# Kernel optimization log

Hardware: AMD Instinct MI355X
Metric: run time of the kernel (lower is better)

Reference implementation:

```python
import jax, jax.numpy as jnp
import numpy as np

NUM_CLASSES = 5
FEATURES = 256      # self.features_num
DIRECTIONS = 10000  # self.directions_num
H = 128
W = 128
LOSS_WEIGHT = 1.0


def setup_inputs() -> dict:
    key = jax.random.key(0)
    k1, k2, k3 = jax.random.split(key, 3)
    feature = jax.random.normal(k1, (1, FEATURES, H, W), dtype=jnp.float32)
    label = jax.random.randint(k2, (1, 1, H, W), 0, NUM_CLASSES, dtype=jnp.int32)
    proj_mat = jax.random.normal(k3, (DIRECTIONS, FEATURES), dtype=jnp.float32)
    # __init__ normalizes each row to unit norm
    proj_mat = proj_mat / jnp.sqrt((proj_mat ** 2).sum(axis=1, keepdims=True))
    return {"feature": feature, "label": label, "proj_mat": proj_mat}


def _class_loss(feat2d, w, proj_mat):
    # feat2d: [F, N] features, w: [N] {0,1} mask for this class, proj_mat: [D, F]
    n = w.sum()
    n_safe = jnp.maximum(n, 1.0)
    # first/second moments over the masked pixels (detached in the original via .cpu().numpy())
    miu = (feat2d @ w) / n_safe                                  # [F]
    m2mat = ((feat2d * w[None, :]) @ feat2d.T) / n_safe          # [F, F]
    cov_eps = jnp.clip(1e-8 * 1000.0 / n_safe, 1e-8, 1e-5)
    cov = m2mat - jnp.outer(miu, miu) + cov_eps * jnp.eye(FEATURES, dtype=feat2d.dtype)
    cov = jax.lax.stop_gradient(cov)  # original computes eig on detached numpy cov
    evals, evecs = jnp.linalg.eigh(cov)  # cov symmetric -> eigh (original: np.linalg.eig + sort)
    order = jnp.argsort(evals)[::-1]
    evals = jnp.maximum(evals[order], 1e-12)
    evecs = evecs[:, order]
    # per-direction variance after projection; rows of proj_mat already unit norm
    pm = proj_mat / jnp.sqrt((proj_mat ** 2).sum(axis=1, keepdims=True))
    std = jnp.sqrt((pm ** 2) @ evals)                            # [D]
    centered = feat2d - jax.lax.stop_gradient(miu)[:, None]      # miu_curr_t is detached
    # feat_vecs = proj_mat @ (evecs.T @ centered) / std  -> [D, N], the big intermediate
    fp = ((pm @ evecs.T) @ centered) / std[:, None]
    # masked moment accumulation (only class pixels contribute)
    m2 = ((fp ** 2) @ w) / n_safe                                # [D]
    m4 = ((fp ** 4) @ w) / n_safe                                # [D]
    loss_m2 = jnp.mean((m2 - 1.0) ** 2)
    loss_kurt = jnp.mean((m4 - 3.0 * m2 ** 2) ** 2)  # Gaussian target: m4 = 3*m2^2
    active = (n > 0).astype(feat2d.dtype)
    return loss_m2, loss_kurt, active


def reference(feature, label, proj_mat):
    feat2d = feature[0].reshape(FEATURES, H * W)    # [F, N]
    lbl = label[0, 0].reshape(H * W)                # [N]
    total = jnp.zeros((), dtype=feature.dtype)
    active_num = jnp.zeros((), dtype=feature.dtype)
    for c in range(1, NUM_CLASSES):  # original skips class 0 (background)
        w = (lbl == c).astype(feature.dtype)
        lm2, lk, a = _class_loss(feat2d, w, proj_mat)
        total = total + a * (lm2 + lk)
        active_num = active_num + a
    return LOSS_WEIGHT * total / jnp.maximum(active_num, 1.0)
```

## Files before the change

kernel.cpp:

```cpp
#include <hip/hip_runtime.h>
#include <cstdint>
#include <cstddef>

#define FEAT 256
#define HWPX 16384
#define NDIR 10000
#define NCLS 4
#define BCAP 4096
#define NSWO 7
#define JTOL 4e-12f
#define NBLK_FP 157
#define NRND (NSWO*63)

static const size_t OFF_FEATT = 0;
static const size_t OFF_IDX   = OFF_FEATT + (size_t)HWPX*FEAT;
static const size_t OFF_CNT   = OFF_IDX + (size_t)NCLS*HWPX;
static const size_t OFF_MIU   = OFF_CNT + 64;
static const size_t OFF_MIUP  = OFF_MIU + (size_t)NCLS*FEAT;
static const size_t OFF_G     = OFF_MIUP + (size_t)32*NCLS*FEAT;
static const size_t OFF_ETS   = OFF_G + (size_t)NCLS*FEAT*FEAT;
static const size_t OFF_EVAL  = OFF_ETS + (size_t)NCLS*FEAT*FEAT;
static const size_t OFF_LPART = OFF_EVAL + (size_t)NCLS*FEAT;
static const size_t OFF_B     = OFF_LPART + (size_t)NCLS*160*2;
static const size_t OFF_XCH   = OFF_B + (size_t)NCLS*FEAT*BCAP;

#define XCH_STRIDE  ((size_t)131072)
#define XCH_PIN_OFF 65536
#define XCH_FLG_OFF (65536 + 1024)

__device__ __forceinline__ float wsum64(float v){
  int x;
  x = __builtin_amdgcn_update_dpp(0, __float_as_int(v), 0x121, 0xF, 0xF, false); v += __int_as_float(x);
  x = __builtin_amdgcn_update_dpp(0, __float_as_int(v), 0x122, 0xF, 0xF, false); v += __int_as_float(x);
  x = __builtin_amdgcn_update_dpp(0, __float_as_int(v), 0x124, 0xF, 0xF, false); v += __int_as_float(x);
  x = __builtin_amdgcn_update_dpp(0, __float_as_int(v), 0x128, 0xF, 0xF, false); v += __int_as_float(x);
  float a = __int_as_float(__builtin_amdgcn_readlane(__float_as_int(v), 0));
  float b = __int_as_float(__builtin_amdgcn_readlane(__float_as_int(v), 16));
  float c = __int_as_float(__builtin_amdgcn_readlane(__float_as_int(v), 32));
  float d = __int_as_float(__builtin_amdgcn_readlane(__float_as_int(v), 48));
  return (a + b) + (c + d);
}

__device__ __forceinline__ void sysst(float* p, float v){
  __hip_atomic_store(p, v, __ATOMIC_RELAXED, __HIP_MEMORY_SCOPE_SYSTEM);
}
__device__ __forceinline__ float sysld(const float* p){
  return __hip_atomic_load(p, __ATOMIC_RELAXED, __HIP_MEMORY_SCOPE_SYSTEM);
}
__device__ __forceinline__ void syssti(int* p, int v){
  __hip_atomic_store(p, v, __ATOMIC_RELAXED, __HIP_MEMORY_SCOPE_SYSTEM);
}
__device__ __forceinline__ int sysldi(const int* p){
  return __hip_atomic_load(p, __ATOMIC_RELAXED, __HIP_MEMORY_SCOPE_SYSTEM);
}
__device__ __forceinline__ void waitflag(int* f, int val){
  while (sysldi(f) < val) __builtin_amdgcn_s_sleep(1);
  asm volatile("" ::: "memory");
}

__global__ __launch_bounds__(256) void k_transpose(const float* __restrict__ feat, float* __restrict__ ws){
  __shared__ float tile[32][33];
  float* featT = ws + OFF_FEATT;
  int j0 = blockIdx.x*32, f0 = blockIdx.y*32;
  int tx = threadIdx.x, ty = threadIdx.y;
  #pragma unroll
  for (int r=0;r<4;r++){
    int f = f0 + ty + r*8;
    tile[ty+r*8][tx] = feat[(size_t)f*HWPX + j0 + tx];
  }
  __syncthreads();
  #pragma unroll
  for (int r=0;r<4;r++){
    int j = j0 + ty + r*8;
    featT[(size_t)j*FEAT + f0 + tx] = tile[tx][ty+r*8];
  }
}

__global__ __launch_bounds__(256) void k_index(const int* __restrict__ lab, float* ws){
  __shared__ int sc[256];
  int* idx = (int*)(ws + OFF_IDX);
  int* cnt = (int*)(ws + OFF_CNT);
  int t = threadIdx.x;
  if (t < 160){
    #pragma unroll
    for (int cc=0; cc<NCLS; cc++){
      int* fb = (int*)(ws + OFF_XCH + (size_t)cc*XCH_STRIDE + XCH_FLG_OFF);
      fb[t] = 0;
    }
  }
  int base = t*64;
  for (int c=1;c<=NCLS;c++){
    __syncthreads();
    int m = 0;
    for (int k=0;k<64;k++) m += (lab[base+k]==c) ? 1 : 0;
    sc[t] = m;
    __syncthreads();
    for (int off=1; off<256; off<<=1){
      int v = (t>=off)? sc[t-off] : 0;
      __syncthreads();
      sc[t] += v;
      __syncthreads();
    }
    int pos = sc[t] - m;
    if (t==255) cnt[c-1] = sc[255];
    int* ic = idx + (size_t)(c-1)*HWPX;
    for (int k=0;k<64;k++){
      if (lab[base+k]==c) ic[pos++] = base+k;
    }
  }
}

__global__ __launch_bounds__(256) void k_miu_part(const int* __restrict__ lab, float* ws){
  const float* featT = ws + OFF_FEATT;
  float* part = ws + OFF_MIUP;
  int f = threadIdx.x;
  int b = blockIdx.x;
  int j0 = b*512;
  float a0=0.f,a1=0.f,a2=0.f,a3=0.f;
  for (int j=j0;j<j0+512;j++){
    float v = featT[(size_t)j*FEAT + f];
    int c = lab[j];
    a0 += (c==1)? v : 0.f;
    a1 += (c==2)? v : 0.f;
    a2 += (c==3)? v : 0.f;
    a3 += (c==4)? v : 0.f;
  }
  float* pb = part + (size_t)b*NCLS*FEAT;
  pb[0*FEAT+f] = a0;
  pb[1*FEAT+f] = a1;
  pb[2*FEAT+f] = a2;
  pb[3*FEAT+f] = a3;
}

__global__ __launch_bounds__(1024) void k_miu_fin(float* ws){
  int t = threadIdx.x;
  int c = t / FEAT;
  const float* part = ws + OFF_MIUP;
  float s = 0.f;
  for (int b=0;b<32;b++) s += part[(size_t)b*NCLS*FEAT + t];
  int n = ((int*)(ws+OFF_CNT))[c];
  float nf = fmaxf((float)n, 1.f);
  ws[OFF_MIU + t] = s / nf;
}

__global__ __launch_bounds__(256) void k_cov(float* ws){
  __shared__ float Xa[32][68];
  __shared__ float Xb[32][68];
  const float* featT = ws + OFF_FEATT;
  int c = blockIdx.y;
  const int* idx = (const int*)(ws + OFF_IDX) + (size_t)c*HWPX;
  int n = ((int*)(ws+OFF_CNT))[c];
  float nf = fmaxf((float)n,1.f);
  const float* miu = ws + OFF_MIU + (size_t)c*FEAT;
  float* G = ws + OFF_G + (size_t)c*FEAT*FEAT;
  int fb = (blockIdx.x & 3)*64, gb = (blockIdx.x >> 2)*64;
  int t = threadIdx.x;
  int ti = t & 15, tj = t >> 4;
  float acc[4][4] = {};
  int jr = t >> 3;
  int s8 = (t & 7) * 8;
  int nch = (n + 31)/32;
  for (int ch=0; ch<nch; ch++){
    int jg = ch*32 + jr;
    __syncthreads();
    if (jg < n){
      int jx = idx[jg];
      const float* row = featT + (size_t)jx*FEAT;
      #pragma unroll
      for (int k=0;k<8;k++){ Xa[jr][s8+k] = row[fb+s8+k]; Xb[jr][s8+k] = row[gb+s8+k]; }
    } else {
      #pragma unroll
      for (int k=0;k<8;k++){ Xa[jr][s8+k] = 0.f; Xb[jr][s8+k] = 0.f; }
    }
    __syncthreads();
    for (int jj=0;jj<32;jj++){
      float4 av = *(const float4*)&Xa[jj][ti*4];
      float4 bv = *(const float4*)&Xb[jj][tj*4];
      float aa[4] = {av.x,av.y,av.z,av.w};
      float bb[4] = {bv.x,bv.y,bv.z,bv.w};
      #pragma unroll
      for (int ii=0; ii<4; ii++)
        #pragma unroll
        for (int j2=0; j2<4; j2++)
          acc[ii][j2] += aa[ii]*bb[j2];
    }
  }
  float eps = fminf(fmaxf(1e-5f/nf, 1e-8f), 1e-5f);
  #pragma unroll
  for (int ii=0; ii<4; ii++){
    #pragma unroll
    for (int j2=0; j2<4; j2++){
      int f = fb + ti*4 + ii, g = gb + tj*4 + j2;
      float v = acc[ii][j2]/nf - miu[f]*miu[g] + ((f==g)? eps : 0.f);
      G[(size_t)g*FEAT + f] = v;
    }
  }
}

__global__ __launch_bounds__(64) void k_jacobi(float* ws){
  int c = blockIdx.y;
  int w = blockIdx.x;
  float* G    = ws + OFF_G + (size_t)c*FEAT*FEAT;
  float* XC   = ws + OFF_XCH + (size_t)c*XCH_STRIDE;
  float* QIN  = XC;
  float* PIN  = XC + XCH_PIN_OFF;
  float* csqg = XC + XCH_PIN_OFF;
  int*   flg  = (int*)(XC + XCH_FLG_OFF);
  int* dP = flg;       int* crP = flg+32;
  int* dQ = flg+64;    int* crQ = flg+96;
  int* bar = flg+128;
  int lane = threadIdx.x;
  int lane4 = lane*4;

#define FORJ8(M) M(0) M(1) M(2) M(3) M(4) M(5) M(6) M(7)

#define DECL(j) float C##j##x, C##j##y, C##j##z, C##j##w;
  FORJ8(DECL)
#undef DECL
  float n0,n1,n2,n3,n4,n5,n6,n7;

  int pg = (w==0)? 63 : w;
  int qg = (w==0)? 0  : 63 - w;

#define LDP(j) { float4 v_ = *(const float4*)&G[(size_t)(pg*4+(j))*FEAT + lane4]; \
                 C##j##x=v_.x; C##j##y=v_.y; C##j##z=v_.z; C##j##w=v_.w; }
  LDP(0) LDP(1) LDP(2) LDP(3)
#undef LDP
#define LDQ(j) { float4 v_ = *(const float4*)&G[(size_t)(qg*4+((j)-4))*FEAT + lane4]; \
                 C##j##x=v_.x; C##j##y=v_.y; C##j##z=v_.z; C##j##w=v_.w; }
  LDQ(4) LDQ(5) LDQ(6) LDQ(7)
#undef LDQ

#define RG(g,ax,ay,az,aw)  ax=C##g##x; ay=C##g##y; az=C##g##z; aw=C##g##w;
#define WRG(g,ax,ay,az,aw) C##g##x=ax; C##g##y=ay; C##g##z=az; C##g##w=aw;
#define NRM(j) n##j = wsum64(C##j##x*C##j##x + C##j##y*C##j##y + C##j##z*C##j##z + C##j##w*C##j##w);

#define ROTG(ga,gb) { \
    float ax,ay,az,aw,bx,by,bz,bw; \
    RG(ga,ax,ay,az,aw) \
    RG(gb,bx,by,bz,bw) \
    float dp = ax*bx + ay*by + az*bz + aw*bw; \
    float d = wsum64(dp); \
    float na = n##ga, nb = n##gb; \
    bool doit = (d*d > na*nb*JTOL); \
    float tau = (nb - na) * 0.5f * __builtin_amdgcn_rcpf(d); \
    float tt = copysignf(__builtin_amdgcn_rcpf(fabsf(tau) + __builtin_amdgcn_sqrtf(1.f + tau*tau)), tau); \
    float cc = __builtin_amdgcn_rsqf(1.f + tt*tt); \
    float sn = tt*cc; \
    cc = doit ? cc : 1.f; \
    sn = doit ? sn : 0.f; \
    float x_; \
    x_ = ax; ax = cc*x_ - sn*bx; bx = sn*x_ + cc*bx; \
    x_ = ay; ay = cc*x_ - sn*by; by = sn*x_ + cc*by; \
    x_ = az; az = cc*x_ - sn*bz; bz = sn*x_ + cc*bz; \
    x_ = aw; aw = cc*x_ - sn*bw; bw = sn*x_ + cc*bw; \
    float cc2 = cc*cc, sn2 = sn*sn, csd = 2.f*cc*sn*d; \
    n##ga = cc2*na - csd + sn2*nb; \
    n##gb = sn2*na + csd + cc2*nb; \
    WRG(ga,ax,ay,az,aw) \
    WRG(gb,bx,by,bz,bw) \
  }

#define STC(d_, j) { float* p_ = (d_) + ((j)&3)*256 + lane4; \
    sysst(p_+0, C##j##x); sysst(p_+1, C##j##y); sysst(p_+2, C##j##z); sysst(p_+3, C##j##w); }
#define LDC(s_, j) { const float* p_ = (s_) + ((j)&3)*256 + lane4; \
    C##j##x=sysld(p_+0); C##j##y=sysld(p_+1); C##j##z=sysld(p_+2); C##j##w=sysld(p_+3); }

  bool hasP = (w>=1 && w<=30);
  float* pubPdst = (w==1)? QIN : PIN + (size_t)(w-1)*2048;
  int*   pubPd   = (w==1)? (dQ+0) : (dP+(w-1));
  int*   pubPcr  = (w==1)? (crQ+0) : (crP+(w-1));

#pragma clang loop unroll(disable)
  for (int R=0; R<NRND; R++){
    NRM(0) NRM(1) NRM(2) NRM(3) NRM(4) NRM(5) NRM(6) NRM(7)
    ROTG(0,4) ROTG(1,5) ROTG(2,6) ROTG(3,7)
    ROTG(0,5) ROTG(1,6) ROTG(2,7) ROTG(3,4)
    ROTG(0,6) ROTG(1,7) ROTG(2,4) ROTG(3,5)
    ROTG(0,7) ROTG(1,4) ROTG(2,5) ROTG(3,6)
    if ((R & 3) == 3){
      ROTG(3,0) ROTG(1,2)  ROTG(7,4) ROTG(5,6)
      ROTG(3,1) ROTG(2,0)  ROTG(7,5) ROTG(6,4)
      ROTG(3,2) ROTG(0,1)  ROTG(7,6) ROTG(4,5)
    }

    int sl = (R+1) & 1;
    if (w >= 1) waitflag(pubPcr, R-1);
    if (w <= 30) waitflag(crQ+(w+1), R-1);
    if (w >= 1){
      float* db = pubPdst + sl*1024;
      STC(db,0) STC(db,1) STC(db,2) STC(db,3)
    }
    if (w <= 30){
      float* db = QIN + (size_t)(w+1)*2048 + sl*1024;
      STC(db,4) STC(db,5) STC(db,6) STC(db,7)
    }
    asm volatile("s_waitcnt vmcnt(0)" ::: "memory");
    if (w >= 1) syssti(pubPd, R+1);
    if (w <= 30) syssti(dQ+(w+1), R+1);
    if (w == 31){
      C0x=C4x; C0y=C4y; C0z=C4z; C0w=C4w;
      C1x=C5x; C1y=C5y; C1z=C5z; C1w=C5w;
      C2x=C6x; C2y=C6y; C2z=C6z; C2w=C6w;
      C3x=C7x; C3y=C7y; C3z=C7z; C3w=C7w;
    }
    if (hasP) waitflag(dP+w, R+1);
    waitflag(dQ+w, R+1);
    if (hasP){
      const float* sb = PIN + (size_t)w*2048 + sl*1024;
      LDC(sb,0) LDC(sb,1) LDC(sb,2) LDC(sb,3)
    }
    {
      const float* sb = QIN + (size_t)w*2048 + sl*1024;
      LDC(sb,4) LDC(sb,5) LDC(sb,6) LDC(sb,7)
    }
    asm volatile("s_waitcnt vmcnt(0)" ::: "memory");
    if (hasP) syssti(crP+w, R+1);
    syssti(crQ+w, R+1);
  }

  NRM(0) NRM(1) NRM(2) NRM(3) NRM(4) NRM(5) NRM(6) NRM(7)
  int pcol = pg*4, qcol = qg*4;
#define WCSP(j) if (lane == (j)) sysst(&csqg[pcol+(j)], n##j);
#define WCSQ(j) if (lane == (j)) sysst(&csqg[qcol+(j)-4], n##j);
  WCSP(0) WCSP(1) WCSP(2) WCSP(3) WCSQ(4) WCSQ(5) WCSQ(6) WCSQ(7)
#undef WCSP
#undef WCSQ
  asm volatile("s_waitcnt vmcnt(0)" ::: "memory");
  if (lane == 0) __hip_atomic_fetch_add(bar, 1, __ATOMIC_RELAXED, __HIP_MEMORY_SCOPE_SYSTEM);
  while (sysldi(bar) < 32) __builtin_amdgcn_s_sleep(1);
  asm volatile("" ::: "memory");
  float q0 = sysld(&csqg[lane4+0]);
  float q1 = sysld(&csqg[lane4+1]);
  float q2 = sysld(&csqg[lane4+2]);
  float q3 = sysld(&csqg[lane4+3]);
  int u0 = lane4, u1 = lane4+1, u2 = lane4+2, u3 = lane4+3;
  float* evals = ws + OFF_EVAL + (size_t)c*FEAT;
  float* Et = ws + OFF_ETS + (size_t)c*FEAT*FEAT;
#define RANKWR(j, X) { \
    float nv = n##j; \
    float cnt = (((q0>nv)||(q0==nv&&u0<(X)))?1.f:0.f) + (((q1>nv)||(q1==nv&&u1<(X)))?1.f:0.f) \
              + (((q2>nv)||(q2==nv&&u2<(X)))?1.f:0.f) + (((q3>nv)||(q3==nv&&u3<(X)))?1.f:0.f); \
    int rk = (int)wsum64(cnt); \
    if (lane == 0) evals[rk] = sqrtf(nv); \
    float iv = 1.f / sqrtf(nv); \
    float4 v_; v_.x=C##j##x*iv; v_.y=C##j##y*iv; v_.z=C##j##z*iv; v_.w=C##j##w*iv; \
    *(float4*)&Et[(size_t)rk*FEAT + lane4] = v_; \
  }
  RANKWR(0, pcol+0) RANKWR(1, pcol+1) RANKWR(2, pcol+2) RANKWR(3, pcol+3)
  RANKWR(4, qcol+0) RANKWR(5, qcol+1) RANKWR(6, qcol+2) RANKWR(7, qcol+3)
#undef RANKWR
#undef ROTG
#undef NRM
#undef RG
#undef WRG
#undef STC
#undef LDC
#undef FORJ8
}

__global__ __launch_bounds__(256) void k_bmat(float* ws){
  __shared__ float Ae[256][68];
  __shared__ float Bc[256][68];
  int c = blockIdx.z;
  int n = ((int*)(ws+OFF_CNT))[c];
  int j0 = blockIdx.x*64;
  if (j0 >= n) return;
  int kb = blockIdx.y*64;
  const float* featT = ws + OFF_FEATT;
  const int* idx = (const int*)(ws + OFF_IDX) + (size_t)c*HWPX;
  const float* miu = ws + OFF_MIU + (size_t)c*FEAT;
  const float* Ets = ws + OFF_ETS + (size_t)c*FEAT*FEAT;
  float* Bg = ws + OFF_B + (size_t)c*FEAT*BCAP;
  int t = threadIdx.x;
  int l4 = t >> 2, sgf = (t & 3)*64;
  {
    const float* Erow = Ets + (size_t)(kb+l4)*FEAT + sgf;
    for (int f=0; f<64; f+=4){
      float4 v = *(const float4*)&Erow[f];
      Ae[sgf+f+0][l4] = v.x; Ae[sgf+f+1][l4] = v.y;
      Ae[sgf+f+2][l4] = v.z; Ae[sgf+f+3][l4] = v.w;
    }
  }
  {
    int jg = j0 + l4;
    if (jg < n){
      const float* Frow = featT + (size_t)idx[jg]*FEAT + sgf;
      const float* mp = miu + sgf;
      for (int f=0; f<64; f+=4){
        float4 v = *(const float4*)&Frow[f];
        Bc[sgf+f+0][l4] = v.x - mp[f+0];
        Bc[sgf+f+1][l4] = v.y - mp[f+1];
        Bc[sgf+f+2][l4] = v.z - mp[f+2];
        Bc[sgf+f+3][l4] = v.w - mp[f+3];
      }
    } else {
      for (int f=0; f<64; f++) Bc[sgf+f][l4] = 0.f;
    }
  }
  __syncthreads();
  int ti = t & 15, tj = t >> 4;
  float acc[4][4] = {};
  for (int f=0; f<FEAT; f+=4){
    #pragma unroll
    for (int ff=0; ff<4; ff++){
      float4 av = *(const float4*)&Ae[f+ff][ti*4];
      float4 bv = *(const float4*)&Bc[f+ff][tj*4];
      float aa[4] = {av.x,av.y,av.z,av.w};
      float bb[4] = {bv.x,bv.y,bv.z,bv.w};
      #pragma unroll
      for (int kk=0;kk<4;kk++)
        #pragma unroll
        for (int jj=0;jj<4;jj++)
          acc[kk][jj] += aa[kk]*bb[jj];
    }
  }
  #pragma unroll
  for (int kk=0; kk<4; kk++){
    float4 o; o.x=acc[kk][0]; o.y=acc[kk][1]; o.z=acc[kk][2]; o.w=acc[kk][3];
    *(float4*)&Bg[(size_t)(kb + ti*4 + kk)*BCAP + j0 + tj*4] = o;
  }
}

__global__ __launch_bounds__(256) void k_fp(const float* __restrict__ pm, float* ws){
  __shared__ float As[256][68];
  __shared__ float Bs[256][68];
  __shared__ float ev[256];
  __shared__ float red[64][17];
  __shared__ float m2s[64];
  __shared__ float m4s[64];
  int c = blockIdx.y;
  int i0 = blockIdx.x*64;
  int n = ((int*)(ws+OFF_CNT))[c];
  float nf = fmaxf((float)n, 1.f);
  const float* evals = ws + OFF_EVAL + (size_t)c*FEAT;
  const float* Bg = ws + OFF_B + (size_t)c*FEAT*BCAP;
  int t = threadIdx.x;
  int l4 = t >> 2;
  {
    int sgf = (t & 3)*64;
    int gi = i0 + l4;
    if (gi < NDIR){
      const float* row = pm + (size_t)gi*FEAT + sgf;
      for (int f=0; f<64; f+=4){
        float4 v = *(const float4*)&row[f];
        As[sgf+f+0][l4] = v.x; As[sgf+f+1][l4] = v.y;
        As[sgf+f+2][l4] = v.z; As[sgf+f+3][l4] = v.w;
      }
    } else {
      for (int f=0; f<64; f++) As[sgf+f][l4] = 0.f;
    }
  }
  if (t < 256) ev[t] = evals[t];
  int ti = t & 15, tj = t >> 4;
  float s2[4] = {0.f,0.f,0.f,0.f};
  float s4[4] = {0.f,0.f,0.f,0.f};
  int nch = (n + 63)/64;
  int sgj = (t & 3)*16;
  for (int ch=0; ch<nch; ch++){
    int j0 = ch*64;
    __syncthreads();
    for (int g=0; g<4; g++){
      int r = l4 + 64*g;
      const float* Brow = Bg + (size_t)r*BCAP + j0 + sgj;
      #pragma unroll
      for (int e=0; e<16; e+=4){
        int j = j0 + sgj + e;
        float4 v;
        if (j + 3 < n) v = *(const float4*)&Brow[e];
        else {
          v.x = (j+0<n)? Brow[e+0] : 0.f;
          v.y = (j+1<n)? Brow[e+1] : 0.f;
          v.z = (j+2<n)? Brow[e+2] : 0.f;
          v.w = (j+3<n)? Brow[e+3] : 0.f;
        }
        *(float4*)&Bs[r][sgj+e] = v;
      }
    }
    __syncthreads();
    float acc[4][4] = {};
    for (int k=0; k<FEAT; k+=4){
      #pragma unroll
      for (int kk=0; kk<4; kk++){
        float4 av = *(const float4*)&As[k+kk][ti*4];
        float4 bv = *(const float4*)&Bs[k+kk][tj*4];
        float aa[4] = {av.x,av.y,av.z,av.w};
        float bb[4] = {bv.x,bv.y,bv.z,bv.w};
        #pragma unroll
        for (int ii=0;ii<4;ii++)
          #pragma unroll
          for (int jj=0;jj<4;jj++)
            acc[ii][jj] += aa[ii]*bb[jj];
      }
    }
    #pragma unroll
    for (int ii=0;ii<4;ii++){
      #pragma unroll
      for (int jj=0;jj<4;jj++){
        float v = acc[ii][jj];
        float v2 = v*v;
        s2[ii] += v2;
        s4[ii] += v2*v2;
      }
    }
  }
  __syncthreads();
  #pragma unroll
  for (int ii=0;ii<4;ii++) red[ti*4+ii][tj] = s2[ii];
  __syncthreads();
  if (t < 64){
    float s = 0.f;
    for (int u=0;u<16;u++) s += red[t][u];
    m2s[t] = s;
  }
  __syncthreads();
  #pragma unroll
  for (int ii=0;ii<4;ii++) red[ti*4+ii][tj] = s4[ii];
  __syncthreads();
  if (t < 64){
    float s = 0.f;
    for (int u=0;u<16;u++) s += red[t][u];
    m4s[t] = s;
  }
  __syncthreads();
  if (t < 64){
    float stds = 0.f;
    for (int k=0;k<FEAT;k++){
      float a = As[k][t];
      stds += a*a*ev[k];
    }
    int i = i0 + t;
    float l2 = 0.f, lk = 0.f;
    if (i < NDIR){
      float m2 = m2s[t]/(nf*stds);
      float m4 = m4s[t]/(nf*stds*stds);
      float d2 = m2 - 1.f;
      l2 = d2*d2;
      float dk = m4 - 3.f*m2*m2;
      lk = dk*dk;
    }
    #pragma unroll
    for (int o=1;o<64;o<<=1){
      l2 += __shfl_xor(l2, o);
      lk += __shfl_xor(lk, o);
    }
    if (t == 0){
      float* lp = ws + OFF_LPART + ((size_t)c*160 + blockIdx.x)*2;
      lp[0] = l2;
      lp[1] = lk;
    }
  }
}

__global__ __launch_bounds__(64) void k_final(float* ws, float* out){
  int t = threadIdx.x;
  const int* cnt = (const int*)(ws + OFF_CNT);
  const float* lp = ws + OFF_LPART;
  float tot = 0.f, an = 0.f;
  for (int c=0;c<NCLS;c++){
    float s2 = 0.f, sk = 0.f;
    for (int b=t; b<NBLK_FP; b+=64){
      s2 += lp[((size_t)c*160 + b)*2 + 0];
      sk += lp[((size_t)c*160 + b)*2 + 1];
    }
    #pragma unroll
    for (int o=1;o<64;o<<=1){
      s2 += __shfl_xor(s2, o);
      sk += __shfl_xor(sk, o);
    }
    if (cnt[c] > 0){
      tot += s2/(float)NDIR + sk/(float)NDIR;
      an += 1.f;
    }
  }
  if (t == 0) out[0] = tot / fmaxf(an, 1.f);
}

extern "C" void kernel_launch(void* const* d_in, const int* in_sizes, int n_in,
                              void* d_out, int out_size, void* d_ws, size_t ws_size,
                              hipStream_t stream) {
  const float* feat = (const float*)d_in[0];
  const int*   lab  = (const int*)d_in[1];
  const float* pm   = (const float*)d_in[2];
  float* out = (float*)d_out;
  float* ws  = (float*)d_ws;

  hipLaunchKernelGGL(k_transpose, dim3(HWPX/32, FEAT/32), dim3(32,8), 0, stream, feat, ws);
  hipLaunchKernelGGL(k_index,     dim3(1),            dim3(256),     0, stream, lab, ws);
  hipLaunchKernelGGL(k_miu_part,  dim3(32),           dim3(256),     0, stream, lab, ws);
  hipLaunchKernelGGL(k_miu_fin,   dim3(1),            dim3(1024),    0, stream, ws);
  hipLaunchKernelGGL(k_cov,       dim3(16, NCLS),     dim3(256),     0, stream, ws);
  hipLaunchKernelGGL(k_jacobi,    dim3(32, NCLS),     dim3(64),      0, stream, ws);
  hipLaunchKernelGGL(k_bmat,      dim3(BCAP/64, 4, NCLS), dim3(256), 0, stream, ws);
  hipLaunchKernelGGL(k_fp,        dim3(NBLK_FP, NCLS), dim3(256),    0, stream, pm, ws);
  hipLaunchKernelGGL(k_final,     dim3(1),            dim3(64),      0, stream, ws, out);
}
```

Measured before the change: 4.676 ms.

## Use 8-column groups per wave in one-sided Jacobi, halving inter-block exchange rounds

Restructures the distributed one-sided Jacobi eigen-solver so each wave holds 16 columns (8 per group) instead of 8, cutting the wave count per class from 32 to 16 and the rounds per sweep from 63 to 31. Each round now does four times as many intra-wave rotations but half as many cross-block flag handshakes and exchanges through global memory. Atomic scopes also drop from system to agent, which should make the spin-wait loads and stores cheaper. The cost is more register pressure (64 column floats per lane) and fewer blocks working in parallel.

```diff
diff --git a/kernel.cpp b/kernel.cpp
--- a/kernel.cpp
+++ b/kernel.cpp
@@ -10,7 +10,7 @@
 #define NSWO 7
 #define JTOL 4e-12f
 #define NBLK_FP 157
-#define NRND (NSWO*63)
+#define NRND (NSWO*31)
 
 static const size_t OFF_FEATT = 0;
 static const size_t OFF_IDX   = OFF_FEATT + (size_t)HWPX*FEAT;
@@ -42,16 +42,16 @@
 }
 
 __device__ __forceinline__ void sysst(float* p, float v){
-  __hip_atomic_store(p, v, __ATOMIC_RELAXED, __HIP_MEMORY_SCOPE_SYSTEM);
+  __hip_atomic_store(p, v, __ATOMIC_RELAXED, __HIP_MEMORY_SCOPE_AGENT);
 }
 __device__ __forceinline__ float sysld(const float* p){
-  return __hip_atomic_load(p, __ATOMIC_RELAXED, __HIP_MEMORY_SCOPE_SYSTEM);
+  return __hip_atomic_load(p, __ATOMIC_RELAXED, __HIP_MEMORY_SCOPE_AGENT);
 }
 __device__ __forceinline__ void syssti(int* p, int v){
-  __hip_atomic_store(p, v, __ATOMIC_RELAXED, __HIP_MEMORY_SCOPE_SYSTEM);
+  __hip_atomic_store(p, v, __ATOMIC_RELAXED, __HIP_MEMORY_SCOPE_AGENT);
 }
 __device__ __forceinline__ int sysldi(const int* p){
-  return __hip_atomic_load(p, __ATOMIC_RELAXED, __HIP_MEMORY_SCOPE_SYSTEM);
+  return __hip_atomic_load(p, __ATOMIC_RELAXED, __HIP_MEMORY_SCOPE_AGENT);
 }
 __device__ __forceinline__ void waitflag(int* f, int val){
   while (sysldi(f) < val) __builtin_amdgcn_s_sleep(1);
@@ -81,7 +81,7 @@
   int* idx = (int*)(ws + OFF_IDX);
   int* cnt = (int*)(ws + OFF_CNT);
   int t = threadIdx.x;
-  if (t < 160){
+  if (t < 96){
     #pragma unroll
     for (int cc=0; cc<NCLS; cc++){
       int* fb = (int*)(ws + OFF_XCH + (size_t)cc*XCH_STRIDE + XCH_FLG_OFF);
@@ -206,29 +206,30 @@
   float* PIN  = XC + XCH_PIN_OFF;
   float* csqg = XC + XCH_PIN_OFF;
   int*   flg  = (int*)(XC + XCH_FLG_OFF);
-  int* dP = flg;       int* crP = flg+32;
-  int* dQ = flg+64;    int* crQ = flg+96;
-  int* bar = flg+128;
+  int* dP = flg;       int* crP = flg+16;
+  int* dQ = flg+32;    int* crQ = flg+48;
+  int* bar = flg+64;
   int lane = threadIdx.x;
   int lane4 = lane*4;
 
-#define FORJ8(M) M(0) M(1) M(2) M(3) M(4) M(5) M(6) M(7)
+#define FORJ8L(M) M(0) M(1) M(2) M(3) M(4) M(5) M(6) M(7)
+#define FORJ8H(M) M(8) M(9) M(10) M(11) M(12) M(13) M(14) M(15)
 
 #define DECL(j) float C##j##x, C##j##y, C##j##z, C##j##w;
-  FORJ8(DECL)
+  FORJ8L(DECL) FORJ8H(DECL)
 #undef DECL
-  float n0,n1,n2,n3,n4,n5,n6,n7;
-
-  int pg = (w==0)? 63 : w;
-  int qg = (w==0)? 0  : 63 - w;
-
-#define LDP(j) { float4 v_ = *(const float4*)&G[(size_t)(pg*4+(j))*FEAT + lane4]; \
+  float n0,n1,n2,n3,n4,n5,n6,n7,n8,n9,n10,n11,n12,n13,n14,n15;
+
+  int pg = (w==0)? 31 : w;
+  int qg = (w==0)? 0  : 31 - w;
+
+#define LDP(j) { float4 v_ = *(const float4*)&G[(size_t)(pg*8+(j))*FEAT + lane4]; \
                  C##j##x=v_.x; C##j##y=v_.y; C##j##z=v_.z; C##j##w=v_.w; }
-  LDP(0) LDP(1) LDP(2) LDP(3)
+  FORJ8L(LDP)
 #undef LDP
-#define LDQ(j) { float4 v_ = *(const float4*)&G[(size_t)(qg*4+((j)-4))*FEAT + lane4]; \
+#define LDQ(j) { float4 v_ = *(const float4*)&G[(size_t)(qg*8+((j)-8))*FEAT + lane4]; \
                  C##j##x=v_.x; C##j##y=v_.y; C##j##z=v_.z; C##j##w=v_.w; }
-  LDQ(4) LDQ(5) LDQ(6) LDQ(7)
+  FORJ8H(LDQ)
 #undef LDQ
 
 #define RG(g,ax,ay,az,aw)  ax=C##g##x; ay=C##g##y; az=C##g##z; aw=C##g##w;
@@ -261,58 +262,71 @@
     WRG(gb,bx,by,bz,bw) \
   }
 
-#define STC(d_, j) { float* p_ = (d_) + ((j)&3)*256 + lane4; \
+#define STC(d_, j) { float* p_ = (d_) + ((j)&7)*256 + lane4; \
     sysst(p_+0, C##j##x); sysst(p_+1, C##j##y); sysst(p_+2, C##j##z); sysst(p_+3, C##j##w); }
-#define LDC(s_, j) { const float* p_ = (s_) + ((j)&3)*256 + lane4; \
+#define LDC(s_, j) { const float* p_ = (s_) + ((j)&7)*256 + lane4; \
     C##j##x=sysld(p_+0); C##j##y=sysld(p_+1); C##j##z=sysld(p_+2); C##j##w=sysld(p_+3); }
 
-  bool hasP = (w>=1 && w<=30);
-  float* pubPdst = (w==1)? QIN : PIN + (size_t)(w-1)*2048;
+  bool hasP = (w>=1 && w<=14);
+  float* pubPdst = (w==1)? QIN : PIN + (size_t)(w-1)*4096;
   int*   pubPd   = (w==1)? (dQ+0) : (dP+(w-1));
   int*   pubPcr  = (w==1)? (crQ+0) : (crP+(w-1));
 
 #pragma clang loop unroll(disable)
   for (int R=0; R<NRND; R++){
     NRM(0) NRM(1) NRM(2) NRM(3) NRM(4) NRM(5) NRM(6) NRM(7)
-    ROTG(0,4) ROTG(1,5) ROTG(2,6) ROTG(3,7)
-    ROTG(0,5) ROTG(1,6) ROTG(2,7) ROTG(3,4)
-    ROTG(0,6) ROTG(1,7) ROTG(2,4) ROTG(3,5)
-    ROTG(0,7) ROTG(1,4) ROTG(2,5) ROTG(3,6)
+    NRM(8) NRM(9) NRM(10) NRM(11) NRM(12) NRM(13) NRM(14) NRM(15)
+    ROTG(0,8)  ROTG(1,9)  ROTG(2,10) ROTG(3,11) ROTG(4,12) ROTG(5,13) ROTG(6,14) ROTG(7,15)
+    ROTG(0,9)  ROTG(1,10) ROTG(2,11) ROTG(3,12) ROTG(4,13) ROTG(5,14) ROTG(6,15) ROTG(7,8)
+    ROTG(0,10) ROTG(1,11) ROTG(2,12) ROTG(3,13) ROTG(4,14) ROTG(5,15) ROTG(6,8)  ROTG(7,9)
+    ROTG(0,11) ROTG(1,12) ROTG(2,13) ROTG(3,14) ROTG(4,15) ROTG(5,8)  ROTG(6,9)  ROTG(7,10)
+    ROTG(0,12) ROTG(1,13) ROTG(2,14) ROTG(3,15) ROTG(4,8)  ROTG(5,9)  ROTG(6,10) ROTG(7,11)
+    ROTG(0,13) ROTG(1,14) ROTG(2,15) ROTG(3,8)  ROTG(4,9)  ROTG(5,10) ROTG(6,11) ROTG(7,12)
+    ROTG(0,14) ROTG(1,15) ROTG(2,8)  ROTG(3,9)  ROTG(4,10) ROTG(5,11) ROTG(6,12) ROTG(7,13)
+    ROTG(0,15) ROTG(1,8)  ROTG(2,9)  ROTG(3,10) ROTG(4,11) ROTG(5,12) ROTG(6,13) ROTG(7,14)
     if ((R & 3) == 3){
-      ROTG(3,0) ROTG(1,2)  ROTG(7,4) ROTG(5,6)
-      ROTG(3,1) ROTG(2,0)  ROTG(7,5) ROTG(6,4)
-      ROTG(3,2) ROTG(0,1)  ROTG(7,6) ROTG(4,5)
+      ROTG(7,0) ROTG(1,6) ROTG(2,5) ROTG(3,4)  ROTG(15,8)  ROTG(9,14)  ROTG(10,13) ROTG(11,12)
+      ROTG(7,1) ROTG(2,0) ROTG(3,6) ROTG(4,5)  ROTG(15,9)  ROTG(10,8)  ROTG(11,14) ROTG(12,13)
+      ROTG(7,2) ROTG(3,1) ROTG(4,0) ROTG(5,6)  ROTG(15,10) ROTG(11,9)  ROTG(12,8)  ROTG(13,14)
+      ROTG(7,3) ROTG(4,2) ROTG(5,1) ROTG(6,0)  ROTG(15,11) ROTG(12,10) ROTG(13,9)  ROTG(14,8)
+      ROTG(7,4) ROTG(5,3) ROTG(6,2) ROTG(0,1)  ROTG(15,12) ROTG(13,11) ROTG(14,10) ROTG(8,9)
+      ROTG(7,5) ROTG(6,4) ROTG(0,3) ROTG(1,2)  ROTG(15,13) ROTG(14,12) ROTG(8,11)  ROTG(9,10)
+      ROTG(7,6) ROTG(0,5) ROTG(1,4) ROTG(2,3)  ROTG(15,14) ROTG(8,13)  ROTG(9,12)  ROTG(10,11)
     }
 
     int sl = (R+1) & 1;
     if (w >= 1) waitflag(pubPcr, R-1);
-    if (w <= 30) waitflag(crQ+(w+1), R-1);
+    if (w <= 14) waitflag(crQ+(w+1), R-1);
     if (w >= 1){
-      float* db = pubPdst + sl*1024;
-      STC(db,0) STC(db,1) STC(db,2) STC(db,3)
-    }
-    if (w <= 30){
-      float* db = QIN + (size_t)(w+1)*2048 + sl*1024;
-      STC(db,4) STC(db,5) STC(db,6) STC(db,7)
+      float* db = pubPdst + sl*2048;
+      STC(db,0) STC(db,1) STC(db,2) STC(db,3) STC(db,4) STC(db,5) STC(db,6) STC(db,7)
+    }
+    if (w <= 14){
+      float* db = QIN + (size_t)(w+1)*4096 + sl*2048;
+      STC(db,8) STC(db,9) STC(db,10) STC(db,11) STC(db,12) STC(db,13) STC(db,14) STC(db,15)
     }
     asm volatile("s_waitcnt vmcnt(0)" ::: "memory");
     if (w >= 1) syssti(pubPd, R+1);
-    if (w <= 30) syssti(dQ+(w+1), R+1);
-    if (w == 31){
-      C0x=C4x; C0y=C4y; C0z=C4z; C0w=C4w;
-      C1x=C5x; C1y=C5y; C1z=C5z; C1w=C5w;
-      C2x=C6x; C2y=C6y; C2z=C6z; C2w=C6w;
-      C3x=C7x; C3y=C7y; C3z=C7z; C3w=C7w;
+    if (w <= 14) syssti(dQ+(w+1), R+1);
+    if (w == 15){
+      C0x=C8x;  C0y=C8y;  C0z=C8z;  C0w=C8w;
+      C1x=C9x;  C1y=C9y;  C1z=C9z;  C1w=C9w;
+      C2x=C10x; C2y=C10y; C2z=C10z; C2w=C10w;
+      C3x=C11x; C3y=C11y; C3z=C11z; C3w=C11w;
+      C4x=C12x; C4y=C12y; C4z=C12z; C4w=C12w;
+      C5x=C13x; C5y=C13y; C5z=C13z; C5w=C13w;
+      C6x=C14x; C6y=C14y; C6z=C14z; C6w=C14w;
+      C7x=C15x; C7y=C15y; C7z=C15z; C7w=C15w;
     }
     if (hasP) waitflag(dP+w, R+1);
     waitflag(dQ+w, R+1);
     if (hasP){
-      const float* sb = PIN + (size_t)w*2048 + sl*1024;
-      LDC(sb,0) LDC(sb,1) LDC(sb,2) LDC(sb,3)
+      const float* sb = PIN + (size_t)w*4096 + sl*2048;
+      LDC(sb,0) LDC(sb,1) LDC(sb,2) LDC(sb,3) LDC(sb,4) LDC(sb,5) LDC(sb,6) LDC(sb,7)
     }
     {
-      const float* sb = QIN + (size_t)w*2048 + sl*1024;
-      LDC(sb,4) LDC(sb,5) LDC(sb,6) LDC(sb,7)
+      const float* sb = QIN + (size_t)w*4096 + sl*2048;
+      LDC(sb,8) LDC(sb,9) LDC(sb,10) LDC(sb,11) LDC(sb,12) LDC(sb,13) LDC(sb,14) LDC(sb,15)
     }
     asm volatile("s_waitcnt vmcnt(0)" ::: "memory");
     if (hasP) syssti(crP+w, R+1);
@@ -320,15 +334,17 @@
   }
 
   NRM(0) NRM(1) NRM(2) NRM(3) NRM(4) NRM(5) NRM(6) NRM(7)
-  int pcol = pg*4, qcol = qg*4;
+  NRM(8) NRM(9) NRM(10) NRM(11) NRM(12) NRM(13) NRM(14) NRM(15)
+  int pcol = pg*8, qcol = qg*8;
 #define WCSP(j) if (lane == (j)) sysst(&csqg[pcol+(j)], n##j);
-#define WCSQ(j) if (lane == (j)) sysst(&csqg[qcol+(j)-4], n##j);
-  WCSP(0) WCSP(1) WCSP(2) WCSP(3) WCSQ(4) WCSQ(5) WCSQ(6) WCSQ(7)
+#define WCSQ(j) if (lane == (j)) sysst(&csqg[qcol+(j)-8], n##j);
+  WCSP(0) WCSP(1) WCSP(2) WCSP(3) WCSP(4) WCSP(5) WCSP(6) WCSP(7)
+  WCSQ(8) WCSQ(9) WCSQ(10) WCSQ(11) WCSQ(12) WCSQ(13) WCSQ(14) WCSQ(15)
 #undef WCSP
 #undef WCSQ
   asm volatile("s_waitcnt vmcnt(0)" ::: "memory");
-  if (lane == 0) __hip_atomic_fetch_add(bar, 1, __ATOMIC_RELAXED, __HIP_MEMORY_SCOPE_SYSTEM);
-  while (sysldi(bar) < 32) __builtin_amdgcn_s_sleep(1);
+  if (lane == 0) __hip_atomic_fetch_add(bar, 1, __ATOMIC_RELAXED, __HIP_MEMORY_SCOPE_AGENT);
+  while (sysldi(bar) < 16) __builtin_amdgcn_s_sleep(1);
   asm volatile("" ::: "memory");
   float q0 = sysld(&csqg[lane4+0]);
   float q1 = sysld(&csqg[lane4+1]);
@@ -347,8 +363,10 @@
     float4 v_; v_.x=C##j##x*iv; v_.y=C##j##y*iv; v_.z=C##j##z*iv; v_.w=C##j##w*iv; \
     *(float4*)&Et[(size_t)rk*FEAT + lane4] = v_; \
   }
-  RANKWR(0, pcol+0) RANKWR(1, pcol+1) RANKWR(2, pcol+2) RANKWR(3, pcol+3)
-  RANKWR(4, qcol+0) RANKWR(5, qcol+1) RANKWR(6, qcol+2) RANKWR(7, qcol+3)
+  RANKWR(0,  pcol+0) RANKWR(1,  pcol+1) RANKWR(2,  pcol+2) RANKWR(3,  pcol+3)
+  RANKWR(4,  pcol+4) RANKWR(5,  pcol+5) RANKWR(6,  pcol+6) RANKWR(7,  pcol+7)
+  RANKWR(8,  qcol+0) RANKWR(9,  qcol+1) RANKWR(10, qcol+2) RANKWR(11, qcol+3)
+  RANKWR(12, qcol+4) RANKWR(13, qcol+5) RANKWR(14, qcol+6) RANKWR(15, qcol+7)
 #undef RANKWR
 #undef ROTG
 #undef NRM
@@ -356,7 +374,8 @@
 #undef WRG
 #undef STC
 #undef LDC
-#undef FORJ8
+#undef FORJ8L
+#undef FORJ8H
 }
 
 __global__ __launch_bounds__(256) void k_bmat(float* ws){
@@ -590,7 +609,7 @@
   hipLaunchKernelGGL(k_miu_part,  dim3(32),           dim3(256),     0, stream, lab, ws);
   hipLaunchKernelGGL(k_miu_fin,   dim3(1),            dim3(1024),    0, stream, ws);
   hipLaunchKernelGGL(k_cov,       dim3(16, NCLS),     dim3(256),     0, stream, ws);
-  hipLaunchKernelGGL(k_jacobi,    dim3(32, NCLS),     dim3(64),      0, stream, ws);
+  hipLaunchKernelGGL(k_jacobi,    dim3(16, NCLS),     dim3(64),      0, stream, ws);
   hipLaunchKernelGGL(k_bmat,      dim3(BCAP/64, 4, NCLS), dim3(256), 0, stream, ws);
   hipLaunchKernelGGL(k_fp,        dim3(NBLK_FP, NCLS), dim3(256),    0, stream, pm, ws);
   hipLaunchKernelGGL(k_final,     dim3(1),            dim3(64),      0, stream, ws, out);
```

Measured after the change: 4.918 ms. 1.05x slower.
